# Kernel tuning notes

Measured on AMD Instinct MI355X. Metric: run time of the kernel, lower is better.

Reference implementation:

```python
import jax, jax.numpy as jnp
import numpy as np

N_NODES = 100000
N_EDGES = 3200000
IN_DIM = 128
HID = 64
N_GRAPHS = 64
BN_EPS = 1e-5


def setup_inputs() -> dict:
    key = jax.random.key(0)
    ks = jax.random.split(key, 12)
    x = jax.random.normal(ks[0], (N_NODES, IN_DIM), dtype=jnp.float32)
    edge_index = jax.random.randint(ks[1], (2, N_EDGES), 0, N_NODES, dtype=jnp.int64)
    edge_weight = jax.random.uniform(ks[2], (N_EDGES,), dtype=jnp.float32)
    batch = jnp.sort(jax.random.randint(ks[3], (N_NODES,), 0, N_GRAPHS, dtype=jnp.int64))
    s1 = 1.0 / np.sqrt(IN_DIM)
    s2 = 1.0 / np.sqrt(HID)
    W1 = jax.random.uniform(ks[4], (IN_DIM, HID), jnp.float32, -s1, s1)
    b1 = jnp.zeros((HID,), jnp.float32)
    W2 = jax.random.uniform(ks[5], (HID, HID), jnp.float32, -s2, s2)
    b2 = jnp.zeros((HID,), jnp.float32)
    g1 = jnp.ones((HID,), jnp.float32)
    be1 = jnp.zeros((HID,), jnp.float32)
    g2 = jnp.ones((HID,), jnp.float32)
    be2 = jnp.zeros((HID,), jnp.float32)
    Wout = jax.random.uniform(ks[6], (HID, 1), jnp.float32, -s2, s2)
    bout = jnp.zeros((1,), jnp.float32)
    return {"x": x, "edge_index": edge_index, "edge_weight": edge_weight,
            "batch": batch, "W1": W1, "b1": b1, "W2": W2, "b2": b2,
            "g1": g1, "be1": be1, "g2": g2, "be2": be2,
            "Wout": Wout, "bout": bout}


def _gcn_norm(edge_index, edge_weight, n_nodes):
    """Add self-loops and compute symmetric GCN normalization coefficients."""
    loop = jnp.arange(n_nodes, dtype=edge_index.dtype)
    row = jnp.concatenate([edge_index[0], loop])   # source nodes
    col = jnp.concatenate([edge_index[1], loop])   # target nodes
    w = jnp.concatenate([edge_weight, jnp.ones((n_nodes,), edge_weight.dtype)])
    deg = jax.ops.segment_sum(w, col, num_segments=n_nodes)
    dinv = jnp.where(deg > 0, jax.lax.rsqrt(jnp.where(deg > 0, deg, 1.0)), 0.0)
    norm = dinv[row] * w * dinv[col]
    return row, col, norm


def _gcn_layer(h, row, col, norm, W, b, n_nodes):
    h = h @ W                                             # [N, H]
    msg = h[row] * norm[:, None]                          # gather + scale
    agg = jax.ops.segment_sum(msg, col, num_segments=n_nodes)  # scatter-add
    return agg + b


def _batchnorm(h, gamma, beta):
    mean = jnp.mean(h, axis=0)
    var = jnp.mean(jnp.square(h - mean), axis=0)
    return gamma * (h - mean) * jax.lax.rsqrt(var + BN_EPS) + beta


def reference(x, edge_index, edge_weight, batch, W1, b1, W2, b2,
              g1, be1, g2, be2, Wout, bout):
    n = x.shape[0]
    row, col, norm = _gcn_norm(edge_index, edge_weight, n)
    # layer 1: GCNConv -> BN -> ReLU (dropout = identity in eval)
    h = _gcn_layer(x, row, col, norm, W1, b1, n)
    h = jax.nn.relu(_batchnorm(h, g1, be1))
    # layer 2
    h = _gcn_layer(h, row, col, norm, W2, b2, n)
    h = jax.nn.relu(_batchnorm(h, g2, be2))
    # global mean pool over graphs
    sums = jax.ops.segment_sum(h, batch, num_segments=N_GRAPHS)
    counts = jax.ops.segment_sum(jnp.ones((n,), h.dtype), batch, num_segments=N_GRAPHS)
    pooled = sums / jnp.maximum(counts, 1.0)[:, None]
    return pooled @ Wout + bout
```

## Files before the change

### kernel.cpp

```cpp
#include <hip/hip_runtime.h>
#include <stdint.h>

#define N_NODES 100000
#define N_EDGES 3200000
#define IN_DIM 128
#define HID 64
#define N_GRAPHS 64
#define BN_EPS 1e-5f
#define NSHARD 16
#define BUCK_SH 7
#define BUCK_SZ 128
#define NBUCK ((N_NODES + BUCK_SZ - 1) / BUCK_SZ)
#define NCNT (NBUCK * 8)
#define BINB_EDGES 4096
#define BIN_BLOCKS ((N_EDGES + BINB_EDGES - 1) / BINB_EDGES)
#define SLOT_CAP 768
#define BCAP 4608
#define SORT_CAP (8 * SLOT_CAP)
#define AGG_CAP 2048

typedef float vf4 __attribute__((ext_vector_type(4)));
typedef int   vi4 __attribute__((ext_vector_type(4)));
typedef unsigned vu2 __attribute__((ext_vector_type(2)));
typedef _Float16 vh4 __attribute__((ext_vector_type(4)));

__device__ __forceinline__ float4 nt_f4(const float* p) {
    vf4 v = __builtin_nontemporal_load((const vf4*)p);
    return make_float4(v.x, v.y, v.z, v.w);
}
__device__ __forceinline__ int4 nt_i4(const int* p) {
    vi4 v = __builtin_nontemporal_load((const vi4*)p);
    return make_int4(v.x, v.y, v.z, v.w);
}
__device__ __forceinline__ uint2 nt_u2(const uint2* p) {
    vu2 v = __builtin_nontemporal_load((const vu2*)p);
    return make_uint2(v.x, v.y);
}
__device__ __forceinline__ vh4 nt_h4(const _Float16* p) {
    return __builtin_nontemporal_load((const vh4*)p);
}

__global__ void k_init(int* __restrict__ cur) {
    int i = blockIdx.x * blockDim.x + threadIdx.x;
    if (i < NCNT) cur[i] = i * SLOT_CAP;
}

__global__ __launch_bounds__(512) void k_bin(const int* __restrict__ ei,
                                             const float* __restrict__ ew,
                                             int* __restrict__ cur,
                                             uint2* __restrict__ ebuf) {
    __shared__ int hist[NBUCK];
    int b = blockIdx.x, t = threadIdx.x;
    int s = b & 7;
    int base = b * BINB_EDGES;
    int n = min(BINB_EDGES, N_EDGES - base);
    for (int i = t; i < NBUCK; i += 512) hist[i] = 0;
    __syncthreads();
#pragma unroll
    for (int k = 0; k < 2; ++k) {
        int ch = t + 512 * k;
        if (4 * ch < n) {
            int4 c4 = nt_i4(ei + N_EDGES + base + 4 * ch);
            atomicAdd(&hist[c4.x >> BUCK_SH], 1);
            atomicAdd(&hist[c4.y >> BUCK_SH], 1);
            atomicAdd(&hist[c4.z >> BUCK_SH], 1);
            atomicAdd(&hist[c4.w >> BUCK_SH], 1);
        }
    }
    __syncthreads();
    for (int j = t; j < NBUCK; j += 512) {
        int h = hist[j];
        if (h > 0) hist[j] = atomicAdd(&cur[s * NBUCK + j], h);
    }
    __syncthreads();
#pragma unroll
    for (int k = 0; k < 2; ++k) {
        int ch = t + 512 * k;
        if (4 * ch < n) {
            int4 r4 = nt_i4(ei + base + 4 * ch);
            int4 c4 = nt_i4(ei + N_EDGES + base + 4 * ch);
            float4 w4 = nt_f4(ew + base + 4 * ch);
            int rr[4] = {r4.x, r4.y, r4.z, r4.w};
            int cc[4] = {c4.x, c4.y, c4.z, c4.w};
            float ww[4] = {w4.x, w4.y, w4.z, w4.w};
            int pos[4];
#pragma unroll
            for (int u = 0; u < 4; ++u)
                pos[u] = atomicAdd(&hist[cc[u] >> BUCK_SH], 1);
#pragma unroll
            for (int u = 0; u < 4; ++u)
                ebuf[pos[u]] = make_uint2(
                    (unsigned)(rr[u] | ((cc[u] & (BUCK_SZ - 1)) << 17)),
                    __float_as_uint(ww[u]));
        }
    }
}

__global__ __launch_bounds__(512) void k_sortnorm(const uint2* __restrict__ ebuf,
                                                  const int* __restrict__ cur,
                                                  float* __restrict__ dinv,
                                                  uint2* __restrict__ ebuf2,
                                                  int2* __restrict__ nrange) {
    __shared__ uint2 se[SORT_CAP];
    __shared__ float sdi[BUCK_SZ];
    __shared__ int scnt[BUCK_SZ];
    __shared__ int scur[BUCK_SZ];
    __shared__ int slen[8], soffc[8];
    int b = blockIdx.x, t = threadIdx.x;
    if (t < BUCK_SZ) { sdi[t] = 0.f; scnt[t] = 0; }
    if (t < 8) slen[t] = cur[t * NBUCK + b] - (t * NBUCK + b) * SLOT_CAP;
    __syncthreads();
    if (t == 0) {
        int run = 0;
#pragma unroll
        for (int s = 0; s < 8; ++s) { soffc[s] = run; run += slen[s]; }
    }
    __syncthreads();
    for (int s = 0; s < 8; ++s) {
        int sb = (s * NBUCK + b) * SLOT_CAP;
        int len = slen[s];
        int off = soffc[s];
        for (int i = t; i < len; i += 512) {
            uint2 u = nt_u2(ebuf + sb + i);
            se[off + i] = u;
            int cl = u.x >> 17;
            atomicAdd(&sdi[cl], __uint_as_float(u.y));
            atomicAdd(&scnt[cl], 1);
        }
    }
    __syncthreads();
    int n = soffc[7] + slen[7];
    if (t < BUCK_SZ) {
        float di = rsqrtf(sdi[t] + 1.0f);
        int node = b * BUCK_SZ + t;
        if (node < N_NODES) dinv[node] = di;
        sdi[t] = di;
    }
    __syncthreads();
    for (int off = 1; off < BUCK_SZ; off <<= 1) {
        int x = 0;
        if (t < BUCK_SZ && t >= off) x = scnt[t - off];
        __syncthreads();
        if (t < BUCK_SZ) scnt[t] += x;
        __syncthreads();
    }
    if (t < BUCK_SZ) {
        int excl = (t > 0) ? scnt[t - 1] : 0;
        int cnt = scnt[t] - excl;
        scur[t] = b * BCAP + excl;
        int node = b * BUCK_SZ + t;
        if (node < N_NODES) nrange[node] = make_int2(b * BCAP + excl, b * BCAP + excl + cnt);
    }
    __syncthreads();
    for (int i = t; i < n; i += 512) {
        uint2 u = se[i];
        int r = u.x & 131071;
        int cl = u.x >> 17;
        float nm = __uint_as_float(u.y) * sdi[cl];
        int p = atomicAdd(&scur[cl], 1);
        ebuf2[p] = make_uint2((unsigned)r, __float_as_uint(nm));
    }
}

template <int K, bool BNH>
__global__ __launch_bounds__(256) void k_gemm(const void* __restrict__ in_,
                                              const float* __restrict__ W,
                                              const float* __restrict__ scale,
                                              const float* __restrict__ shift,
                                              const float* __restrict__ dinv,
                                              _Float16* __restrict__ out) {
    __shared__ float ws[K * 64];
    __shared__ float xs[32 * 132];
    __shared__ float ssc[64], ssh[64];
    int t = threadIdx.x;
    int nbase = blockIdx.x * 128;

#pragma unroll
    for (int i = 0; i < K / 16; ++i) {
        int idx = t + 256 * i;
        ((float4*)ws)[idx] = ((const float4*)W)[idx];
    }
    if (BNH && t < 64) { ssc[t] = scale[t]; ssh[t] = shift[t]; }

    int cg = t & 15;
    int ng = t >> 4;
    float acc[8][4];
#pragma unroll
    for (int i = 0; i < 8; ++i)
#pragma unroll
        for (int j = 0; j < 4; ++j) acc[i][j] = 0.f;

    for (int k0 = 0; k0 < K; k0 += 32) {
        __syncthreads();
#pragma unroll
        for (int i = 0; i < 4; ++i) {
            int idx = t + 256 * i;
            int row = idx >> 3;
            int kq = idx & 7;
            int node = nbase + row;
            float vv[4] = {0.f, 0.f, 0.f, 0.f};
            if (node < N_NODES) {
                if (BNH) {
                    vh4 v = nt_h4((const _Float16*)in_ + (size_t)node * K + k0 + kq * 4);
                    vv[0] = (float)v.x; vv[1] = (float)v.y;
                    vv[2] = (float)v.z; vv[3] = (float)v.w;
                } else {
                    float4 v = nt_f4((const float*)in_ + (size_t)node * K + k0 + kq * 4);
                    vv[0] = v.x; vv[1] = v.y; vv[2] = v.z; vv[3] = v.w;
                }
            }
#pragma unroll
            for (int u = 0; u < 4; ++u) {
                float val = vv[u];
                if (BNH) {
                    int k = k0 + kq * 4 + u;
                    val = fmaxf(ssc[k] * val + ssh[k], 0.f);
                }
                xs[(kq * 4 + u) * 132 + row] = val;
            }
        }
        __syncthreads();
#pragma unroll
        for (int k = 0; k < 32; ++k) {
            float4 wv = *(const float4*)(ws + (k0 + k) * 64 + cg * 4);
            float4 xa = *(const float4*)(xs + k * 132 + ng * 8);
            float4 xb = *(const float4*)(xs + k * 132 + ng * 8 + 4);
            float xv[8] = {xa.x, xa.y, xa.z, xa.w, xb.x, xb.y, xb.z, xb.w};
            float wvv[4] = {wv.x, wv.y, wv.z, wv.w};
#pragma unroll
            for (int i = 0; i < 8; ++i)
#pragma unroll
                for (int j = 0; j < 4; ++j) acc[i][j] += xv[i] * wvv[j];
        }
    }
#pragma unroll
    for (int i = 0; i < 8; ++i) {
        int node = nbase + ng * 8 + i;
        if (node < N_NODES) {
            float dv = dinv[node];
            vh4 o;
            o.x = (_Float16)(acc[i][0] * dv); o.y = (_Float16)(acc[i][1] * dv);
            o.z = (_Float16)(acc[i][2] * dv); o.w = (_Float16)(acc[i][3] * dv);
            *(vh4*)(out + (size_t)node * 64 + cg * 4) = o;
        }
    }
}

__global__ __launch_bounds__(256) void k_agg(const _Float16* __restrict__ hin,
                                             const uint2* __restrict__ ebuf2,
                                             const int2* __restrict__ nrange,
                                             const float* __restrict__ dinv,
                                             const float* __restrict__ bias,
                                             _Float16* __restrict__ hout,
                                             float* __restrict__ bn_shard) {
    __shared__ uint2 sme[AGG_CAP];
    __shared__ float sm[4][64], qm[4][64];
    int b = blockIdx.x, t = threadIdx.x;
    int wave = t >> 6, lane = t & 63;
    int vbase0 = b * 32;
    int ebeg = nrange[vbase0].x;
    int eend = nrange[vbase0 + 31].y;
    int n = eend - ebeg;
    bool fit = (n <= AGG_CAP);
    if (fit) {
        for (int i = t; i < n; i += 256) sme[i] = nt_u2(ebuf2 + ebeg + i);
    }
    __syncthreads();

    float s = 0.f, q = 0.f;
    float bl = bias[lane];
    int vbase = vbase0 + wave * 8;
    for (int vi = 0; vi < 8; ++vi) {
        int v = vbase + vi;
        int2 be = nrange[v];
        int beg = be.x, end = be.y;
        float acc = 0.f;
        int j = beg;
        if (fit) {
            for (; j + 16 <= end; j += 16) {
                float fv[16], fn[16];
#pragma unroll
                for (int u = 0; u < 16; ++u) {
                    uint2 e = sme[j - ebeg + u];
                    fn[u] = __uint_as_float(e.y);
                    fv[u] = (float)hin[((size_t)e.x << 6) + lane];
                }
#pragma unroll
                for (int u = 0; u < 16; ++u) acc = fmaf(fn[u], fv[u], acc);
            }
            for (; j + 8 <= end; j += 8) {
                float fv[8], fn[8];
#pragma unroll
                for (int u = 0; u < 8; ++u) {
                    uint2 e = sme[j - ebeg + u];
                    fn[u] = __uint_as_float(e.y);
                    fv[u] = (float)hin[((size_t)e.x << 6) + lane];
                }
#pragma unroll
                for (int u = 0; u < 8; ++u) acc = fmaf(fn[u], fv[u], acc);
            }
            for (; j < end; ++j) {
                uint2 e = sme[j - ebeg];
                acc = fmaf(__uint_as_float(e.y),
                           (float)hin[((size_t)e.x << 6) + lane], acc);
            }
        } else {
            for (; j + 8 <= end; j += 8) {
                float fv[8], fn[8];
#pragma unroll
                for (int u = 0; u < 8; ++u) {
                    uint2 e = nt_u2(ebuf2 + j + u);
                    fn[u] = __uint_as_float(e.y);
                    fv[u] = (float)hin[((size_t)e.x << 6) + lane];
                }
#pragma unroll
                for (int u = 0; u < 8; ++u) acc = fmaf(fn[u], fv[u], acc);
            }
            for (; j < end; ++j) {
                uint2 e = nt_u2(ebuf2 + j);
                acc = fmaf(__uint_as_float(e.y),
                           (float)hin[((size_t)e.x << 6) + lane], acc);
            }
        }
        float dv = dinv[v];
        acc = fmaf(dv, (float)hin[((size_t)v << 6) + lane], acc);
        acc += bl;
        hout[((size_t)v << 6) + lane] = (_Float16)acc;
        s += acc;
        q += acc * acc;
    }
    sm[wave][lane] = s;
    qm[wave][lane] = q;
    __syncthreads();
    if (wave == 0) {
        float ts = sm[0][lane] + sm[1][lane] + sm[2][lane] + sm[3][lane];
        float tq = qm[0][lane] + qm[1][lane] + qm[2][lane] + qm[3][lane];
        float* shard = bn_shard + (blockIdx.x & (NSHARD - 1)) * 128;
        atomicAdd(&shard[lane], ts);
        atomicAdd(&shard[64 + lane], tq);
    }
}

__global__ void k_bn_final(float* __restrict__ bn_shard, const float* __restrict__ gamma,
                           const float* __restrict__ beta, float* __restrict__ scale,
                           float* __restrict__ shift) {
    int t = threadIdx.x;
    if (t < 64) {
        float s = 0.f, q = 0.f;
        for (int i = 0; i < NSHARD; ++i) {
            s += bn_shard[i * 128 + t];
            q += bn_shard[i * 128 + 64 + t];
        }
        float mean = s * (1.0f / N_NODES);
        float var = q * (1.0f / N_NODES) - mean * mean;
        float sc = gamma[t] * rsqrtf(var + BN_EPS);
        scale[t] = sc;
        shift[t] = beta[t] - mean * sc;
    }
    __syncthreads();
    for (int i = t; i < NSHARD * 128; i += 256) bn_shard[i] = 0.f;
}

__global__ __launch_bounds__(256) void k_pool(const _Float16* __restrict__ a2,
                                              const float* __restrict__ scale,
                                              const float* __restrict__ shift,
                                              const int* __restrict__ batch,
                                              float* __restrict__ pooled_sh,
                                              float* __restrict__ pcnt_sh) {
    int b = blockIdx.x, t = threadIdx.x;
    int c = t & 63;
    int rg = t >> 6;
    int base = b * BUCK_SZ;
    float sc = scale[c], sh = shift[c];
    float* pool_s = pooled_sh + (size_t)(b & (NSHARD - 1)) * (N_GRAPHS * 64);
    float* pcnt_s = pcnt_sh + (size_t)(b & (NSHARD - 1)) * N_GRAPHS;
    int gcur = -1;
    float acc = 0.f, cacc = 0.f;
    for (int i = rg; i < BUCK_SZ; i += 4) {
        int v = base + i;
        if (v >= N_NODES) break;
        int g = batch[v];
        if (g != gcur) {
            if (gcur >= 0) {
                atomicAdd(&pool_s[gcur * 64 + c], acc);
                if (c == 0) atomicAdd(&pcnt_s[gcur], cacc);
            }
            gcur = g;
            acc = 0.f;
            cacc = 0.f;
        }
        float h = fmaxf(sc * (float)a2[(size_t)v * 64 + c] + sh, 0.f);
        acc += h;
        cacc += 1.f;
    }
    if (gcur >= 0) {
        atomicAdd(&pool_s[gcur * 64 + c], acc);
        if (c == 0) atomicAdd(&pcnt_s[gcur], cacc);
    }
}

__global__ void k_out(const float* __restrict__ pooled_sh,
                      const float* __restrict__ pcnt_sh,
                      const float* __restrict__ Wout, const float* __restrict__ bout,
                      float* __restrict__ out) {
    int g = threadIdx.x;
    if (g < N_GRAPHS) {
        float cnt = 0.f;
        for (int s = 0; s < NSHARD; ++s) cnt += pcnt_sh[s * N_GRAPHS + g];
        cnt = fmaxf(cnt, 1.0f);
        float sum = 0.f;
        for (int c = 0; c < 64; ++c) {
            float p = 0.f;
            for (int s = 0; s < NSHARD; ++s)
                p += pooled_sh[(size_t)s * N_GRAPHS * 64 + g * 64 + c];
            sum += p * Wout[c];
        }
        out[g] = sum / cnt + bout[0];
    }
}

extern "C" void kernel_launch(void* const* d_in, const int* in_sizes, int n_in,
                              void* d_out, int out_size, void* d_ws, size_t ws_size,
                              hipStream_t stream) {
    const float* x    = (const float*)d_in[0];
    const int*   ei   = (const int*)d_in[1];
    const float* ew   = (const float*)d_in[2];
    const int*   batch= (const int*)d_in[3];
    const float* W1   = (const float*)d_in[4];
    const float* b1   = (const float*)d_in[5];
    const float* W2   = (const float*)d_in[6];
    const float* b2   = (const float*)d_in[7];
    const float* g1   = (const float*)d_in[8];
    const float* be1  = (const float*)d_in[9];
    const float* g2   = (const float*)d_in[10];
    const float* be2  = (const float*)d_in[11];
    const float* Wout = (const float*)d_in[12];
    const float* bout = (const float*)d_in[13];
    float* out = (float*)d_out;

    char* w = (char*)d_ws;
    size_t o = 0;
    auto alloc = [&](size_t bytes) -> void* {
        void* p = w + o;
        o = (o + bytes + 255) & ~(size_t)255;
        return p;
    };
    int*   cur     = (int*)alloc(NCNT * 4);
    int2*  nrange  = (int2*)alloc((size_t)N_NODES * 8);
    float* dinv    = (float*)alloc(N_NODES * 4);
    float* bnshard = (float*)alloc(NSHARD * 128 * 4);
    float* scale1  = (float*)alloc(64 * 4);
    float* shift1  = (float*)alloc(64 * 4);
    float* scale2  = (float*)alloc(64 * 4);
    float* shift2  = (float*)alloc(64 * 4);
    float* pooled  = (float*)alloc(NSHARD * N_GRAPHS * 64 * 4);
    float* pcnt    = (float*)alloc(NSHARD * N_GRAPHS * 4);
    uint2* ebuf2   = (uint2*)alloc((size_t)NBUCK * BCAP * 8);
    uint2* ebuf    = (uint2*)alloc((size_t)NCNT * SLOT_CAP * 8);
    _Float16* bufHA = (_Float16*)ebuf;
    _Float16* bufHB = bufHA + (size_t)N_NODES * 64;
    if (o > ws_size) return;

    (void)hipMemsetAsync(bnshard, 0, NSHARD * 128 * 4, stream);
    (void)hipMemsetAsync(pooled, 0, NSHARD * N_GRAPHS * 64 * 4, stream);
    (void)hipMemsetAsync(pcnt, 0, NSHARD * N_GRAPHS * 4, stream);

    k_init<<<(NCNT + 255) / 256, 256, 0, stream>>>(cur);
    k_bin<<<BIN_BLOCKS, 512, 0, stream>>>(ei, ew, cur, ebuf);
    k_sortnorm<<<NBUCK, 512, 0, stream>>>(ebuf, cur, dinv, ebuf2, nrange);

    k_gemm<128, false><<<(N_NODES + 127) / 128, 256, 0, stream>>>(x, W1, nullptr, nullptr, dinv, bufHA);
    k_agg<<<N_NODES / 32, 256, 0, stream>>>(bufHA, ebuf2, nrange, dinv, b1, bufHB, bnshard);
    k_bn_final<<<1, 256, 0, stream>>>(bnshard, g1, be1, scale1, shift1);

    k_gemm<64, true><<<(N_NODES + 127) / 128, 256, 0, stream>>>(bufHB, W2, scale1, shift1, dinv, bufHA);
    k_agg<<<N_NODES / 32, 256, 0, stream>>>(bufHA, ebuf2, nrange, dinv, b2, bufHB, bnshard);
    k_bn_final<<<1, 256, 0, stream>>>(bnshard, g2, be2, scale2, shift2);

    k_pool<<<NBUCK, 256, 0, stream>>>(bufHB, scale2, shift2, batch, pooled, pcnt);
    k_out<<<1, 64, 0, stream>>>(pooled, pcnt, Wout, bout, out);
}
```

Before: 353.1 us.

## Pack CSR edges into 32-bit words with fp16 weight and factor out target dinv

```diff
diff --git a/kernel.cpp b/kernel.cpp
--- a/kernel.cpp
+++ b/kernel.cpp
@@ -36,8 +36,19 @@
     vu2 v = __builtin_nontemporal_load((const vu2*)p);
     return make_uint2(v.x, v.y);
 }
+__device__ __forceinline__ unsigned nt_u(const unsigned* p) {
+    return __builtin_nontemporal_load(p);
+}
 __device__ __forceinline__ vh4 nt_h4(const _Float16* p) {
     return __builtin_nontemporal_load((const vh4*)p);
+}
+
+__device__ __forceinline__ unsigned pack_edge(unsigned r, _Float16 w) {
+    unsigned short hb = __builtin_bit_cast(unsigned short, w);
+    return (r << 15) | (unsigned)hb;
+}
+__device__ __forceinline__ float unpack_w(unsigned u) {
+    return (float)__builtin_bit_cast(_Float16, (unsigned short)(u & 0x7FFFu));
 }
 
 __global__ void k_init(int* __restrict__ cur) {
@@ -99,9 +110,10 @@
 __global__ __launch_bounds__(512) void k_sortnorm(const uint2* __restrict__ ebuf,
                                                   const int* __restrict__ cur,
                                                   float* __restrict__ dinv,
-                                                  uint2* __restrict__ ebuf2,
+                                                  unsigned* __restrict__ ebuf2,
                                                   int2* __restrict__ nrange) {
-    __shared__ uint2 se[SORT_CAP];
+    __shared__ unsigned sex[SORT_CAP];
+    __shared__ _Float16 sew[SORT_CAP];
     __shared__ float sdi[BUCK_SZ];
     __shared__ int scnt[BUCK_SZ];
     __shared__ int scur[BUCK_SZ];
@@ -122,9 +134,11 @@
         int off = soffc[s];
         for (int i = t; i < len; i += 512) {
             uint2 u = nt_u2(ebuf + sb + i);
-            se[off + i] = u;
+            float wf = __uint_as_float(u.y);
+            sex[off + i] = u.x;
+            sew[off + i] = (_Float16)wf;
             int cl = u.x >> 17;
-            atomicAdd(&sdi[cl], __uint_as_float(u.y));
+            atomicAdd(&sdi[cl], wf);
             atomicAdd(&scnt[cl], 1);
         }
     }
@@ -134,7 +148,6 @@
         float di = rsqrtf(sdi[t] + 1.0f);
         int node = b * BUCK_SZ + t;
         if (node < N_NODES) dinv[node] = di;
-        sdi[t] = di;
     }
     __syncthreads();
     for (int off = 1; off < BUCK_SZ; off <<= 1) {
@@ -153,12 +166,11 @@
     }
     __syncthreads();
     for (int i = t; i < n; i += 512) {
-        uint2 u = se[i];
-        int r = u.x & 131071;
-        int cl = u.x >> 17;
-        float nm = __uint_as_float(u.y) * sdi[cl];
+        unsigned x = sex[i];
+        unsigned r = x & 131071u;
+        int cl = x >> 17;
         int p = atomicAdd(&scur[cl], 1);
-        ebuf2[p] = make_uint2((unsigned)r, __float_as_uint(nm));
+        ebuf2[p] = pack_edge(r, sew[i]);
     }
 }
 
@@ -247,13 +259,13 @@
 }
 
 __global__ __launch_bounds__(256) void k_agg(const _Float16* __restrict__ hin,
-                                             const uint2* __restrict__ ebuf2,
+                                             const unsigned* __restrict__ ebuf2,
                                              const int2* __restrict__ nrange,
                                              const float* __restrict__ dinv,
                                              const float* __restrict__ bias,
                                              _Float16* __restrict__ hout,
                                              float* __restrict__ bn_shard) {
-    __shared__ uint2 sme[AGG_CAP];
+    __shared__ unsigned sme[AGG_CAP];
     __shared__ float sm[4][64], qm[4][64];
     int b = blockIdx.x, t = threadIdx.x;
     int wave = t >> 6, lane = t & 63;
@@ -263,7 +275,7 @@
     int n = eend - ebeg;
     bool fit = (n <= AGG_CAP);
     if (fit) {
-        for (int i = t; i < n; i += 256) sme[i] = nt_u2(ebuf2 + ebeg + i);
+        for (int i = t; i < n; i += 256) sme[i] = nt_u(ebuf2 + ebeg + i);
     }
     __syncthreads();
 
@@ -281,9 +293,9 @@
                 float fv[16], fn[16];
 #pragma unroll
                 for (int u = 0; u < 16; ++u) {
-                    uint2 e = sme[j - ebeg + u];
-                    fn[u] = __uint_as_float(e.y);
-                    fv[u] = (float)hin[((size_t)e.x << 6) + lane];
+                    unsigned e = sme[j - ebeg + u];
+                    fn[u] = unpack_w(e);
+                    fv[u] = (float)hin[((size_t)(e >> 15) << 6) + lane];
                 }
 #pragma unroll
                 for (int u = 0; u < 16; ++u) acc = fmaf(fn[u], fv[u], acc);
@@ -292,39 +304,38 @@
                 float fv[8], fn[8];
 #pragma unroll
                 for (int u = 0; u < 8; ++u) {
-                    uint2 e = sme[j - ebeg + u];
-                    fn[u] = __uint_as_float(e.y);
-                    fv[u] = (float)hin[((size_t)e.x << 6) + lane];
+                    unsigned e = sme[j - ebeg + u];
+                    fn[u] = unpack_w(e);
+                    fv[u] = (float)hin[((size_t)(e >> 15) << 6) + lane];
                 }
 #pragma unroll
                 for (int u = 0; u < 8; ++u) acc = fmaf(fn[u], fv[u], acc);
             }
             for (; j < end; ++j) {
-                uint2 e = sme[j - ebeg];
-                acc = fmaf(__uint_as_float(e.y),
-                           (float)hin[((size_t)e.x << 6) + lane], acc);
+                unsigned e = sme[j - ebeg];
+                acc = fmaf(unpack_w(e),
+                           (float)hin[((size_t)(e >> 15) << 6) + lane], acc);
             }
         } else {
             for (; j + 8 <= end; j += 8) {
                 float fv[8], fn[8];
 #pragma unroll
                 for (int u = 0; u < 8; ++u) {
-                    uint2 e = nt_u2(ebuf2 + j + u);
-                    fn[u] = __uint_as_float(e.y);
-                    fv[u] = (float)hin[((size_t)e.x << 6) + lane];
+                    unsigned e = nt_u(ebuf2 + j + u);
+                    fn[u] = unpack_w(e);
+                    fv[u] = (float)hin[((size_t)(e >> 15) << 6) + lane];
                 }
 #pragma unroll
                 for (int u = 0; u < 8; ++u) acc = fmaf(fn[u], fv[u], acc);
             }
             for (; j < end; ++j) {
-                uint2 e = nt_u2(ebuf2 + j);
-                acc = fmaf(__uint_as_float(e.y),
-                           (float)hin[((size_t)e.x << 6) + lane], acc);
-            }
-        }
-        float dv = dinv[v];
-        acc = fmaf(dv, (float)hin[((size_t)v << 6) + lane], acc);
-        acc += bl;
+                unsigned e = nt_u(ebuf2 + j);
+                acc = fmaf(unpack_w(e),
+                           (float)hin[((size_t)(e >> 15) << 6) + lane], acc);
+            }
+        }
+        acc += (float)hin[((size_t)v << 6) + lane];
+        acc = fmaf(dinv[v], acc, bl);
         hout[((size_t)v << 6) + lane] = (_Float16)acc;
         s += acc;
         q += acc * acc;
@@ -455,7 +466,7 @@
     float* shift2  = (float*)alloc(64 * 4);
     float* pooled  = (float*)alloc(NSHARD * N_GRAPHS * 64 * 4);
     float* pcnt    = (float*)alloc(NSHARD * N_GRAPHS * 4);
-    uint2* ebuf2   = (uint2*)alloc((size_t)NBUCK * BCAP * 8);
+    unsigned* ebuf2 = (unsigned*)alloc((size_t)NBUCK * BCAP * 4);
     uint2* ebuf    = (uint2*)alloc((size_t)NCNT * SLOT_CAP * 8);
     _Float16* bufHA = (_Float16*)ebuf;
     _Float16* bufHB = bufHA + (size_t)N_NODES * 64;
```

New measurement: 350.8 us. Within noise of the previous version (-0.6%).
